# Performance work log

Measured on AMD Instinct MI355X. Metric: run time of the kernel, lower is better.

The kernel has to match this reference:

```python
import jax, jax.numpy as jnp
import numpy as np

B, TQ, TV, D = 32, 1024, 1024, 512


def setup_inputs() -> dict:
    key = jax.random.key(0)
    k1, k2, k3, k4 = jax.random.split(key, 4)
    scale = 1.0 / np.sqrt(D)
    return {
        "query": jax.random.normal(k1, (B, TQ, D), dtype=jnp.float32),
        "value": jax.random.normal(k2, (B, TV, D), dtype=jnp.float32),
        "w_weight": jax.random.normal(k3, (D, D), dtype=jnp.float32) * scale,
        "w_bias": jax.random.normal(k4, (D,), dtype=jnp.float32) * scale,
    }


def reference(query, value, w_weight, w_bias):
    # torch Linear: v @ W^T + b  -> keys [B, Tv, D]
    keys = jnp.einsum("bvd,ed->bve", value, w_weight) + w_bias
    # scores [B, Tq, Tv], softmax over Tv (last dim), unscaled as in source
    scores = jnp.einsum("bqd,bvd->bqv", query, keys)
    alignment = jax.nn.softmax(scores, axis=-1)
    context = jnp.einsum("bqv,bvd->bqd", alignment, value)
    context = jnp.concatenate([context, query], axis=-1)  # [B, Tq, 2D]
    alignment_t = jnp.swapaxes(alignment, 1, 2)  # [B, Tv, Tq]
    return context, alignment_t
```

## Files before the change

kernel.cpp:

```cpp
#include <hip/hip_runtime.h>
#include <hip/hip_bf16.h>

#define NB  32
#define NTQ 1024
#define NTV 1024
#define ND  512

typedef float f32x4 __attribute__((ext_vector_type(4)));
typedef float f32x2 __attribute__((ext_vector_type(2)));
typedef __bf16 bf16x8 __attribute__((ext_vector_type(8)));
typedef _Float16 f16x8 __attribute__((ext_vector_type(8)));
typedef unsigned short u16x4 __attribute__((ext_vector_type(4)));
typedef unsigned short u16x8 __attribute__((ext_vector_type(8)));
typedef unsigned int u32x2 __attribute__((ext_vector_type(2)));
typedef unsigned int u32x4 __attribute__((ext_vector_type(4)));

static __device__ __forceinline__ unsigned short f2h(float x) {
  _Float16 h = (_Float16)x;
  return __builtin_bit_cast(unsigned short, h);
}
static __device__ __forceinline__ float h2f(unsigned short u) {
  return (float)__builtin_bit_cast(_Float16, u);
}
static __device__ __forceinline__ unsigned split2(float x) {
  unsigned u = __builtin_bit_cast(unsigned, x);
  unsigned h = u >> 16;
  float hf = __builtin_bit_cast(float, u & 0xffff0000u);
  unsigned l = __builtin_bit_cast(unsigned, x - hf) >> 16;
  return h | (l << 16);
}
static __device__ __forceinline__ f32x4 mfma_bf(bf16x8 a, bf16x8 b, f32x4 c) {
  return __builtin_amdgcn_mfma_f32_16x16x32_bf16(a, b, c, 0, 0, 0);
}
static __device__ __forceinline__ f32x4 mfma_h(f16x8 a, f16x8 b, f32x4 c) {
  return __builtin_amdgcn_mfma_f32_16x16x32_f16(a, b, c, 0, 0, 0);
}
static __device__ __forceinline__ void gload16(const unsigned short* g, unsigned short* l) {
  __builtin_amdgcn_global_load_lds((const __attribute__((address_space(1))) unsigned*)g,
                                   (__attribute__((address_space(3))) unsigned*)l, 16, 0, 0);
}

__global__ __launch_bounds__(256) void k_vt(const float* __restrict__ V,
                                            unsigned short* __restrict__ Vt) {
  int vt = blockIdx.x, dt = blockIdx.y, b = blockIdx.z;
  int t = threadIdx.x;
  __shared__ unsigned short L[64][72];
#pragma unroll
  for (int r = 0; r < 4; ++r) {
    int v = (t >> 4) + r * 16;
    int c4 = (t & 15) * 4;
    f32x4 x = *(const f32x4*)(V + (size_t)(b * NTV + vt * 64 + v) * ND + dt * 64 + c4);
    u16x4 h;
#pragma unroll
    for (int j = 0; j < 4; ++j) h[j] = f2h(x[j]);
    *(u16x4*)&L[v][c4] = h;
  }
  __syncthreads();
#pragma unroll
  for (int r = 0; r < 4; ++r) {
    int d = (t >> 4) + r * 16;
    int v4 = (t & 15) * 4;
    u16x4 o;
#pragma unroll
    for (int i = 0; i < 4; ++i) o[i] = L[v4 + i][d];
    *(u16x4*)(Vt + (size_t)(b * ND + dt * 64 + d) * NTV + vt * 64 + v4) = o;
  }
}

__global__ __launch_bounds__(256) void k_qhalf(const float* __restrict__ Q,
                                               unsigned short* __restrict__ qh) {
  int base = blockIdx.x * 1024 + threadIdx.x;
#pragma unroll
  for (int k = 0; k < 4; ++k) {
    size_t c = (size_t)(base + k * 256) * 4;
    f32x4 x = *(const f32x4*)(Q + c);
    u16x4 h;
#pragma unroll
    for (int j = 0; j < 4; ++j) h[j] = f2h(x[j]);
    *(u16x4*)(qh + c) = h;
  }
}

__global__ __launch_bounds__(256, 2) void k_keys(const float* __restrict__ V,
                                                 const float* __restrict__ W,
                                                 const float* __restrict__ bias,
                                                 unsigned short* __restrict__ kp) {
  int bid = blockIdx.x;
  int swz = (bid & 7) * 128 + (bid >> 3);
  int bm = swz >> 2, bn = swz & 3;
  int t = threadIdx.x, lane = t & 63, w = t >> 6;
  int l15 = lane & 15, g = lane >> 4;
  int wr = (w >> 1) * 64, wc = (w & 1) * 64;
  __shared__ __align__(16) unsigned char SMEM[73728];
  auto Ah = (unsigned short(*)[72])(SMEM);
  auto Al = (unsigned short(*)[72])(SMEM + 18432);
  auto Bh = (unsigned short(*)[72])(SMEM + 36864);
  auto Bl = (unsigned short(*)[72])(SMEM + 55296);
  f32x4 acc[4][4] = {};
  const int row0 = bm * 128, col0 = bn * 128;
  int srow = t >> 4, c4 = (t & 15) * 4;

  f32x4 vreg[8], wreg[8];
#pragma unroll
  for (int r = 0; r < 8; ++r) {
    vreg[r] = *(const f32x4*)(V + (size_t)(row0 + srow + r * 16) * ND + c4);
    wreg[r] = *(const f32x4*)(W + (size_t)(col0 + srow + r * 16) * ND + c4);
  }
  for (int k0 = 0; k0 < ND; k0 += 64) {
    __syncthreads();
#pragma unroll
    for (int r = 0; r < 8; ++r) {
      int row = srow + r * 16;
      u16x4 h, l;
#pragma unroll
      for (int j = 0; j < 4; ++j) {
        unsigned p = split2(vreg[r][j]);
        h[j] = (unsigned short)(p & 0xffffu); l[j] = (unsigned short)(p >> 16);
      }
      *(u16x4*)&Ah[row][c4] = h; *(u16x4*)&Al[row][c4] = l;
#pragma unroll
      for (int j = 0; j < 4; ++j) {
        unsigned p = split2(wreg[r][j]);
        h[j] = (unsigned short)(p & 0xffffu); l[j] = (unsigned short)(p >> 16);
      }
      *(u16x4*)&Bh[row][c4] = h; *(u16x4*)&Bl[row][c4] = l;
    }
    __syncthreads();
    if (k0 + 64 < ND) {
#pragma unroll
      for (int r = 0; r < 8; ++r) {
        vreg[r] = *(const f32x4*)(V + (size_t)(row0 + srow + r * 16) * ND + k0 + 64 + c4);
        wreg[r] = *(const f32x4*)(W + (size_t)(col0 + srow + r * 16) * ND + k0 + 64 + c4);
      }
    }
#pragma unroll
    for (int kk = 0; kk < 2; ++kk) {
      int kof = kk * 32 + g * 8;
      bf16x8 ah[4], al[4], bh[4], bl[4];
#pragma unroll
      for (int i = 0; i < 4; ++i) {
        int ra = wr + i * 16 + l15;
        ah[i] = *(const bf16x8*)&Ah[ra][kof];
        al[i] = *(const bf16x8*)&Al[ra][kof];
        int rb = wc + i * 16 + l15;
        bh[i] = *(const bf16x8*)&Bh[rb][kof];
        bl[i] = *(const bf16x8*)&Bl[rb][kof];
      }
#pragma unroll
      for (int i = 0; i < 4; ++i)
#pragma unroll
        for (int j = 0; j < 4; ++j) {
          acc[i][j] = mfma_bf(ah[i], bh[j], acc[i][j]);
          acc[i][j] = mfma_bf(ah[i], bl[j], acc[i][j]);
          acc[i][j] = mfma_bf(al[i], bh[j], acc[i][j]);
        }
    }
  }
  __syncthreads();
  float* CT = (float*)SMEM;
#pragma unroll
  for (int j = 0; j < 4; ++j) {
    int col_l = wc + j * 16 + l15;
    float bj = bias[col0 + col_l];
#pragma unroll
    for (int i = 0; i < 4; ++i) {
      int rb_l = wr + i * 16 + g * 4;
#pragma unroll
      for (int r = 0; r < 4; ++r) CT[(rb_l + r) * 132 + col_l] = acc[i][j][r] + bj;
    }
  }
  __syncthreads();
#pragma unroll
  for (int it = 0; it < 16; ++it) {
    int idx = it * 256 + t;
    int row = idx >> 5, cc = (idx & 31) * 4;
    f32x4 x = *(const f32x4*)&CT[row * 132 + cc];
    u16x4 h;
#pragma unroll
    for (int j = 0; j < 4; ++j) h[j] = f2h(x[j]);
    *(u16x4*)(kp + (size_t)(row0 + row) * 2048 + col0 + cc) = h;
  }
}

__global__ __launch_bounds__(256, 3) void k_scores(const unsigned short* __restrict__ qh,
                                                   const unsigned short* kp,
                                                   unsigned short* ebase,
                                                   float2* __restrict__ partials) {
  int bid = blockIdx.x;
  int swz = (bid & 7) * 256 + (bid >> 3);
  int b = swz >> 6, rr2 = swz & 63, vt = rr2 >> 3, qt = rr2 & 7;
  int t = threadIdx.x, lane = t & 63, w = t >> 6, g = lane >> 4, l15 = lane & 15;
  int wr = (w >> 1) * 64, wc = (w & 1) * 64;
  __shared__ __align__(16) unsigned char SMEM[36864];
  unsigned short* lds = (unsigned short*)SMEM;
  f32x4 acc[4][4] = {};
  const size_t qrow = (size_t)(b * NTQ + qt * 128);
  const size_t krow = (size_t)(b * NTV + vt * 128);
  int grow = lane >> 3;
  int gcg = lane & 7;

  for (int k0 = 0; k0 < ND; k0 += 64) {
    __syncthreads();
#pragma unroll
    for (int i = 0; i < 4; ++i) {
      int c = i * 4 + w;
      int row = c * 8 + grow;
      int scg = gcg ^ (row & 7);
      gload16(qh + (qrow + row) * 512 + k0 + scg * 8, lds + c * 512);
      gload16(kp + (krow + row) * 2048 + k0 + scg * 8, lds + 8192 + c * 512);
    }
    __syncthreads();
#pragma unroll
    for (int kk = 0; kk < 2; ++kk) {
      f16x8 af[4], bfr[4];
#pragma unroll
      for (int i = 0; i < 4; ++i) {
        int ra = wr + i * 16 + l15;
        int go = ((kk * 4 + g) ^ (ra & 7)) * 8;
        af[i] = *(const f16x8*)(lds + ra * 64 + go);
        int rb = wc + i * 16 + l15;
        int go2 = ((kk * 4 + g) ^ (rb & 7)) * 8;
        bfr[i] = *(const f16x8*)(lds + 8192 + rb * 64 + go2);
      }
#pragma unroll
      for (int i = 0; i < 4; ++i)
#pragma unroll
        for (int j = 0; j < 4; ++j) acc[i][j] = mfma_h(af[i], bfr[j], acc[i][j]);
    }
  }
  __syncthreads();
  auto E2 = (unsigned short(*)[136])(SMEM);
  float* Lm = (float*)(SMEM + 34816);
  float* Ls = (float*)(SMEM + 35840);
#pragma unroll
  for (int i = 0; i < 4; ++i)
#pragma unroll
    for (int r = 0; r < 4; ++r) {
      float m = fmaxf(fmaxf(acc[i][0][r], acc[i][1][r]), fmaxf(acc[i][2][r], acc[i][3][r]));
#pragma unroll
      for (int msk = 1; msk < 16; msk <<= 1) m = fmaxf(m, __shfl_xor(m, msk));
      if (l15 == 0) Lm[(wr + i * 16 + g * 4 + r) * 2 + (w & 1)] = m;
    }
  __syncthreads();
#pragma unroll
  for (int i = 0; i < 4; ++i)
#pragma unroll
    for (int r = 0; r < 4; ++r) {
      int ql = wr + i * 16 + g * 4 + r;
      float mf = fmaxf(Lm[ql * 2], Lm[ql * 2 + 1]);
      float s = 0.f;
#pragma unroll
      for (int j = 0; j < 4; ++j) {
        float e = __expf(acc[i][j][r] - mf);
        s += e;
        E2[ql][wc + j * 16 + l15] = f2h(e);
      }
#pragma unroll
      for (int msk = 1; msk < 16; msk <<= 1) s += __shfl_xor(s, msk);
      if (l15 == 0) Ls[ql * 2 + (w & 1)] = s;
    }
  __syncthreads();
  if (t < 128) {
    float mf = fmaxf(Lm[t * 2], Lm[t * 2 + 1]);
    float lf = Ls[t * 2] + Ls[t * 2 + 1];
    partials[(((size_t)(b * 8 + vt)) << 10) + qt * 128 + t] = make_float2(mf, lf);
  }
#pragma unroll
  for (int it = 0; it < 8; ++it) {
    int idx = it * 256 + t;
    int row = idx >> 4, ch = idx & 15;
    *(u16x8*)(ebase + (size_t)(b * 1024 + qt * 128 + row) * 2048 + 1024 + vt * 128 + ch * 8) =
        *(const u16x8*)&E2[row][ch * 8];
  }
}

__global__ __launch_bounds__(256) void k_combine(const float2* __restrict__ partials,
                                                 float2* __restrict__ stats) {
  int idx = blockIdx.x * 256 + threadIdx.x;
  int b = idx >> 10, q = idx & 1023;
  float2 p[8];
  float M = -3.0e38f;
#pragma unroll
  for (int vt = 0; vt < 8; ++vt) {
    p[vt] = partials[(((size_t)(b * 8 + vt)) << 10) + q];
    M = fmaxf(M, p[vt].x);
  }
  float L = 0.f;
#pragma unroll
  for (int vt = 0; vt < 8; ++vt) L += p[vt].y * __expf(p[vt].x - M);
  stats[idx] = make_float2(M, 1.0f / L);
}

__global__ __launch_bounds__(256, 3) void k_pv(const unsigned short* __restrict__ ebase,
                                               const unsigned short* __restrict__ Vt,
                                               const float2* __restrict__ stats,
                                               const float2* __restrict__ partials,
                                               float* __restrict__ out1) {
  int bid = blockIdx.x;
  int swz = (bid & 7) * 128 + (bid >> 3);
  int b = swz >> 5, qt = (swz >> 2) & 7, dt = swz & 3;
  int t = threadIdx.x, lane = t & 63, w = t >> 6;
  int l15 = lane & 15, g = lane >> 4;
  int wr = (w >> 1) * 64, wc = (w & 1) * 64;
  int q0 = qt * 128, d0 = dt * 128;
  __shared__ __align__(16) unsigned char SMEM[36864];
  auto Ae = (unsigned short(*)[72])(SMEM);
  auto Bv = (unsigned short(*)[72])(SMEM + 18432);
  f32x4 acc[4][4] = {};

  int srow = t >> 3, c8 = (t & 7) * 8;
  float M4[4], iL4[4];
#pragma unroll
  for (int k = 0; k < 4; ++k) {
    float2 st = stats[b * NTQ + q0 + srow + 32 * k];
    M4[k] = st.x; iL4[k] = st.y;
  }
  u16x8 ereg[4], vreg[4];
#pragma unroll
  for (int k = 0; k < 4; ++k) {
    ereg[k] = *(const u16x8*)(ebase + (size_t)(b * 1024 + q0 + srow + 32 * k) * 2048 + 1024 + c8);
    vreg[k] = *(const u16x8*)(Vt + ((size_t)b * ND + d0 + srow + 32 * k) * NTV + c8);
  }
  float sck[4];
  for (int v0 = 0; v0 < NTV; v0 += 64) {
    if ((v0 & 127) == 0) {
      int vt128 = v0 >> 7;
#pragma unroll
      for (int k = 0; k < 4; ++k) {
        float2 p = partials[(((size_t)(b * 8 + vt128)) << 10) + q0 + srow + 32 * k];
        sck[k] = __expf(p.x - M4[k]) * iL4[k];
      }
    }
    __syncthreads();
#pragma unroll
    for (int k = 0; k < 4; ++k) {
      int row = srow + 32 * k;
      u16x8 a;
#pragma unroll
      for (int m = 0; m < 8; ++m) a[m] = f2h(h2f(ereg[k][m]) * sck[k]);
      *(u16x8*)&Ae[row][c8] = a;
      *(u16x8*)&Bv[row][c8] = vreg[k];
    }
    if (v0 + 64 < NTV) {
#pragma unroll
      for (int k = 0; k < 4; ++k) {
        ereg[k] = *(const u16x8*)(ebase + (size_t)(b * 1024 + q0 + srow + 32 * k) * 2048 + 1024 + v0 + 64 + c8);
        vreg[k] = *(const u16x8*)(Vt + ((size_t)b * ND + d0 + srow + 32 * k) * NTV + v0 + 64 + c8);
      }
    }
    __syncthreads();
#pragma unroll
    for (int kk = 0; kk < 2; ++kk) {
      int kof = kk * 32 + g * 8;
      f16x8 af[4], bfr[4];
#pragma unroll
      for (int i = 0; i < 4; ++i) af[i] = *(const f16x8*)&Ae[wr + i * 16 + l15][kof];
#pragma unroll
      for (int j = 0; j < 4; ++j) bfr[j] = *(const f16x8*)&Bv[wc + j * 16 + l15][kof];
#pragma unroll
      for (int i = 0; i < 4; ++i)
#pragma unroll
        for (int j = 0; j < 4; ++j) acc[i][j] = mfma_h(af[i], bfr[j], acc[i][j]);
    }
  }
  float* CT = (float*)SMEM;
#pragma unroll
  for (int h = 0; h < 2; ++h) {
    __syncthreads();
    if ((w >> 1) == h) {
#pragma unroll
      for (int i = 0; i < 4; ++i)
#pragma unroll
        for (int j = 0; j < 4; ++j) {
          int ql = i * 16 + g * 4;
          int dl = wc + j * 16 + l15;
#pragma unroll
          for (int r = 0; r < 4; ++r) CT[(ql + r) * 132 + dl] = acc[i][j][r];
        }
    }
    __syncthreads();
#pragma unroll
    for (int it = 0; it < 8; ++it) {
      int idx = it * 256 + t;
      int row = idx >> 5, c4 = idx & 31;
      *(f32x4*)(out1 + (size_t)(b * NTQ + q0 + h * 64 + row) * 1024 + d0 + c4 * 4) =
          *(const f32x4*)&CT[row * 132 + c4 * 4];
    }
  }
}

__global__ __launch_bounds__(256) void k_alpha(const unsigned short* ebase,
                                               const float* __restrict__ Q,
                                               const float2* __restrict__ stats,
                                               const float2* __restrict__ partials,
                                               float* out2,
                                               float* out1) {
  int bid = blockIdx.x;
  int swz = (bid & 7) * 64 + (bid >> 3);
  int b = swz >> 4, qc = swz & 15;
  int q0 = qc * 64;
  int t = threadIdx.x;
  __shared__ float T[128][68];
  int row = t >> 4, ch = t & 15;
  float M4[4], iL4[4];
#pragma unroll
  for (int k = 0; k < 4; ++k) {
    float2 st = stats[b * NTQ + q0 + row + 16 * k];
    M4[k] = st.x; iL4[k] = st.y;
  }
  for (int vt = 0; vt < 8; ++vt) {
    __syncthreads();
#pragma unroll
    for (int k = 0; k < 4; ++k) {
      int r = row + 16 * k;
      float2 p = partials[(((size_t)(b * 8 + vt)) << 10) + q0 + r];
      float sc = __expf(p.x - M4[k]) * iL4[k];
      u16x8 ev = *(const u16x8*)(ebase + (size_t)(b * 1024 + q0 + r) * 2048 + 1024 + vt * 128 + ch * 8);
#pragma unroll
      for (int m = 0; m < 8; ++m) {
        int v = ch * 8 + m;
        T[v][r ^ (((v >> 3) & 7) << 3)] = h2f(ev[m]) * sc;
      }
    }
    __syncthreads();
#pragma unroll
    for (int it = 0; it < 8; ++it) {
      int idx = it * 256 + t;
      int vr = idx >> 4, c4 = idx & 15;
      int cs = (c4 * 4) ^ (((vr >> 3) & 7) << 3);
      *(f32x4*)(out2 + ((size_t)(b * 1024) + vt * 128 + vr) * 1024 + q0 + c4 * 4) =
          *(const f32x4*)&T[vr][cs];
    }
  }
  __syncthreads();
#pragma unroll
  for (int k = 0; k < 32; ++k) {
    int idx = k * 256 + t;
    int r = idx >> 7, c4 = idx & 127;
    *(f32x4*)(out1 + (size_t)(b * 1024 + q0 + r) * 1024 + 512 + c4 * 4) =
        *(const f32x4*)(Q + (size_t)(b * 1024 + q0 + r) * 512 + c4 * 4);
  }
}

extern "C" void kernel_launch(void* const* d_in, const int* in_sizes, int n_in,
                              void* d_out, int out_size, void* d_ws, size_t ws_size,
                              hipStream_t stream) {
  const float* Q    = (const float*)d_in[0];
  const float* V    = (const float*)d_in[1];
  const float* W    = (const float*)d_in[2];
  const float* bias = (const float*)d_in[3];

  float* out1 = (float*)d_out;
  float* out2 = (float*)d_out + (size_t)NB * NTQ * (2 * ND);

  unsigned short* Vt = (unsigned short*)d_ws;
  float2* stats    = (float2*)((char*)d_ws + 33554432);
  float2* partials = (float2*)((char*)d_ws + 33554432 + 262144);

  unsigned short* kp = (unsigned short*)out1;
  unsigned short* ebase = (unsigned short*)out1;
  unsigned short* qh = (unsigned short*)out2;

  k_vt<<<dim3(16, 8, 32), 256, 0, stream>>>(V, Vt);
  k_qhalf<<<4096, 256, 0, stream>>>(Q, qh);
  k_keys<<<1024, 256, 0, stream>>>(V, W, bias, kp);
  k_scores<<<2048, 256, 0, stream>>>(qh, kp, ebase, partials);
  k_combine<<<128, 256, 0, stream>>>(partials, stats);
  k_pv<<<1024, 256, 0, stream>>>(ebase, Vt, stats, partials, out1);
  k_alpha<<<512, 256, 0, stream>>>(ebase, Q, stats, partials, out2, out1);
}
```

Before: 276.0 us.

## Merge prep kernels, pre-split W once, and stream W/Vt tiles via direct LDS loads

Merges the V-transpose and Q-to-half conversions into one prep kernel, which also pre-splits W into bf16 hi/lo arrays in the workspace. k_keys then loads the W tiles straight into LDS with global_load_lds using an XOR-swizzled layout, so each block no longer repeats the split and register staging. k_pv loads its Vt tiles the same way. This removes a launch, the redundant per-block W conversion and register pressure from staging. In exchange it adds extra workspace traffic and changes the LDS layout.

```diff
diff --git a/kernel.cpp b/kernel.cpp
--- a/kernel.cpp
+++ b/kernel.cpp
@@ -40,49 +40,70 @@
                                    (__attribute__((address_space(3))) unsigned*)l, 16, 0, 0);
 }
 
-__global__ __launch_bounds__(256) void k_vt(const float* __restrict__ V,
-                                            unsigned short* __restrict__ Vt) {
-  int vt = blockIdx.x, dt = blockIdx.y, b = blockIdx.z;
-  int t = threadIdx.x;
+__global__ __launch_bounds__(256) void k_prep(const float* __restrict__ V,
+                                              const float* __restrict__ Q,
+                                              const float* __restrict__ W,
+                                              unsigned short* __restrict__ Vt,
+                                              unsigned short* __restrict__ qh,
+                                              unsigned short* __restrict__ wh,
+                                              unsigned short* __restrict__ wl) {
   __shared__ unsigned short L[64][72];
-#pragma unroll
-  for (int r = 0; r < 4; ++r) {
-    int v = (t >> 4) + r * 16;
-    int c4 = (t & 15) * 4;
-    f32x4 x = *(const f32x4*)(V + (size_t)(b * NTV + vt * 64 + v) * ND + dt * 64 + c4);
-    u16x4 h;
-#pragma unroll
-    for (int j = 0; j < 4; ++j) h[j] = f2h(x[j]);
-    *(u16x4*)&L[v][c4] = h;
-  }
-  __syncthreads();
-#pragma unroll
-  for (int r = 0; r < 4; ++r) {
-    int d = (t >> 4) + r * 16;
-    int v4 = (t & 15) * 4;
-    u16x4 o;
-#pragma unroll
-    for (int i = 0; i < 4; ++i) o[i] = L[v4 + i][d];
-    *(u16x4*)(Vt + (size_t)(b * ND + dt * 64 + d) * NTV + vt * 64 + v4) = o;
-  }
-}
-
-__global__ __launch_bounds__(256) void k_qhalf(const float* __restrict__ Q,
-                                               unsigned short* __restrict__ qh) {
-  int base = blockIdx.x * 1024 + threadIdx.x;
-#pragma unroll
-  for (int k = 0; k < 4; ++k) {
-    size_t c = (size_t)(base + k * 256) * 4;
-    f32x4 x = *(const f32x4*)(Q + c);
-    u16x4 h;
-#pragma unroll
-    for (int j = 0; j < 4; ++j) h[j] = f2h(x[j]);
-    *(u16x4*)(qh + c) = h;
+  int bid = blockIdx.x, t = threadIdx.x;
+  if (bid < 4096) {
+    int vt = bid & 15, dt = (bid >> 4) & 7, b = bid >> 7;
+#pragma unroll
+    for (int r = 0; r < 4; ++r) {
+      int v = (t >> 4) + r * 16;
+      int c4 = (t & 15) * 4;
+      f32x4 x = *(const f32x4*)(V + (size_t)(b * NTV + vt * 64 + v) * ND + dt * 64 + c4);
+      u16x4 h;
+#pragma unroll
+      for (int j = 0; j < 4; ++j) h[j] = f2h(x[j]);
+      *(u16x4*)&L[v][c4] = h;
+    }
+    __syncthreads();
+#pragma unroll
+    for (int r = 0; r < 4; ++r) {
+      int d = (t >> 4) + r * 16;
+      int v4 = (t & 15) * 4;
+      u16x4 o;
+#pragma unroll
+      for (int i = 0; i < 4; ++i) o[i] = L[v4 + i][d];
+      *(u16x4*)(Vt + (size_t)(b * ND + dt * 64 + d) * NTV + vt * 64 + v4) = o;
+    }
+  } else if (bid < 8192) {
+    int base = (bid - 4096) * 1024 + t;
+#pragma unroll
+    for (int k = 0; k < 4; ++k) {
+      size_t c = (size_t)(base + k * 256) * 4;
+      f32x4 x = *(const f32x4*)(Q + c);
+      u16x4 h;
+#pragma unroll
+      for (int j = 0; j < 4; ++j) h[j] = f2h(x[j]);
+      *(u16x4*)(qh + c) = h;
+    }
+  } else {
+    int base = (bid - 8192) * 1024 + t;
+#pragma unroll
+    for (int k = 0; k < 4; ++k) {
+      size_t c = (size_t)(base + k * 256) * 4;
+      f32x4 x = *(const f32x4*)(W + c);
+      u16x4 hi, lo;
+#pragma unroll
+      for (int j = 0; j < 4; ++j) {
+        unsigned p = split2(x[j]);
+        hi[j] = (unsigned short)(p & 0xffffu);
+        lo[j] = (unsigned short)(p >> 16);
+      }
+      *(u16x4*)(wh + c) = hi;
+      *(u16x4*)(wl + c) = lo;
+    }
   }
 }
 
 __global__ __launch_bounds__(256, 2) void k_keys(const float* __restrict__ V,
-                                                 const float* __restrict__ W,
+                                                 const unsigned short* wh,
+                                                 const unsigned short* wl,
                                                  const float* __restrict__ bias,
                                                  unsigned short* __restrict__ kp) {
   int bid = blockIdx.x;
@@ -91,23 +112,31 @@
   int t = threadIdx.x, lane = t & 63, w = t >> 6;
   int l15 = lane & 15, g = lane >> 4;
   int wr = (w >> 1) * 64, wc = (w & 1) * 64;
-  __shared__ __align__(16) unsigned char SMEM[73728];
+  __shared__ __align__(16) unsigned char SMEM[69632];
   auto Ah = (unsigned short(*)[72])(SMEM);
   auto Al = (unsigned short(*)[72])(SMEM + 18432);
-  auto Bh = (unsigned short(*)[72])(SMEM + 36864);
-  auto Bl = (unsigned short(*)[72])(SMEM + 55296);
+  unsigned short* ldsBh = (unsigned short*)(SMEM + 36864);
+  unsigned short* ldsBl = (unsigned short*)(SMEM + 53248);
   f32x4 acc[4][4] = {};
   const int row0 = bm * 128, col0 = bn * 128;
   int srow = t >> 4, c4 = (t & 15) * 4;
-
-  f32x4 vreg[8], wreg[8];
-#pragma unroll
-  for (int r = 0; r < 8; ++r) {
+  int grow = lane >> 3, gcg = lane & 7;
+
+  f32x4 vreg[8];
+#pragma unroll
+  for (int r = 0; r < 8; ++r)
     vreg[r] = *(const f32x4*)(V + (size_t)(row0 + srow + r * 16) * ND + c4);
-    wreg[r] = *(const f32x4*)(W + (size_t)(col0 + srow + r * 16) * ND + c4);
-  }
+
   for (int k0 = 0; k0 < ND; k0 += 64) {
     __syncthreads();
+#pragma unroll
+    for (int i = 0; i < 4; ++i) {
+      int c = i * 4 + w;
+      int row = c * 8 + grow;
+      int scg = gcg ^ (row & 7);
+      gload16(wh + (size_t)(col0 + row) * 512 + k0 + scg * 8, ldsBh + c * 512);
+      gload16(wl + (size_t)(col0 + row) * 512 + k0 + scg * 8, ldsBl + c * 512);
+    }
 #pragma unroll
     for (int r = 0; r < 8; ++r) {
       int row = srow + r * 16;
@@ -118,20 +147,12 @@
         h[j] = (unsigned short)(p & 0xffffu); l[j] = (unsigned short)(p >> 16);
       }
       *(u16x4*)&Ah[row][c4] = h; *(u16x4*)&Al[row][c4] = l;
-#pragma unroll
-      for (int j = 0; j < 4; ++j) {
-        unsigned p = split2(wreg[r][j]);
-        h[j] = (unsigned short)(p & 0xffffu); l[j] = (unsigned short)(p >> 16);
-      }
-      *(u16x4*)&Bh[row][c4] = h; *(u16x4*)&Bl[row][c4] = l;
     }
     __syncthreads();
     if (k0 + 64 < ND) {
 #pragma unroll
-      for (int r = 0; r < 8; ++r) {
+      for (int r = 0; r < 8; ++r)
         vreg[r] = *(const f32x4*)(V + (size_t)(row0 + srow + r * 16) * ND + k0 + 64 + c4);
-        wreg[r] = *(const f32x4*)(W + (size_t)(col0 + srow + r * 16) * ND + k0 + 64 + c4);
-      }
     }
 #pragma unroll
     for (int kk = 0; kk < 2; ++kk) {
@@ -143,8 +164,9 @@
         ah[i] = *(const bf16x8*)&Ah[ra][kof];
         al[i] = *(const bf16x8*)&Al[ra][kof];
         int rb = wc + i * 16 + l15;
-        bh[i] = *(const bf16x8*)&Bh[rb][kof];
-        bl[i] = *(const bf16x8*)&Bl[rb][kof];
+        int go2 = ((kk * 4 + g) ^ (rb & 7)) * 8;
+        bh[i] = *(const bf16x8*)(ldsBh + rb * 64 + go2);
+        bl[i] = *(const bf16x8*)(ldsBl + rb * 64 + go2);
       }
 #pragma unroll
       for (int i = 0; i < 4; ++i)
@@ -196,8 +218,7 @@
   f32x4 acc[4][4] = {};
   const size_t qrow = (size_t)(b * NTQ + qt * 128);
   const size_t krow = (size_t)(b * NTV + vt * 128);
-  int grow = lane >> 3;
-  int gcg = lane & 7;
+  int grow = lane >> 3, gcg = lane & 7;
 
   for (int k0 = 0; k0 < ND; k0 += 64) {
     __syncthreads();
@@ -292,7 +313,7 @@
 }
 
 __global__ __launch_bounds__(256, 3) void k_pv(const unsigned short* __restrict__ ebase,
-                                               const unsigned short* __restrict__ Vt,
+                                               const unsigned short* Vt,
                                                const float2* __restrict__ stats,
                                                const float2* __restrict__ partials,
                                                float* __restrict__ out1) {
@@ -305,22 +326,22 @@
   int q0 = qt * 128, d0 = dt * 128;
   __shared__ __align__(16) unsigned char SMEM[36864];
   auto Ae = (unsigned short(*)[72])(SMEM);
-  auto Bv = (unsigned short(*)[72])(SMEM + 18432);
+  unsigned short* ldsBv = (unsigned short*)(SMEM + 18432);
   f32x4 acc[4][4] = {};
 
   int srow = t >> 3, c8 = (t & 7) * 8;
+  int grow = lane >> 3, gcg = lane & 7;
   float M4[4], iL4[4];
 #pragma unroll
   for (int k = 0; k < 4; ++k) {
     float2 st = stats[b * NTQ + q0 + srow + 32 * k];
     M4[k] = st.x; iL4[k] = st.y;
   }
-  u16x8 ereg[4], vreg[4];
-#pragma unroll
-  for (int k = 0; k < 4; ++k) {
+  u16x8 ereg[4];
+#pragma unroll
+  for (int k = 0; k < 4; ++k)
     ereg[k] = *(const u16x8*)(ebase + (size_t)(b * 1024 + q0 + srow + 32 * k) * 2048 + 1024 + c8);
-    vreg[k] = *(const u16x8*)(Vt + ((size_t)b * ND + d0 + srow + 32 * k) * NTV + c8);
-  }
+
   float sck[4];
   for (int v0 = 0; v0 < NTV; v0 += 64) {
     if ((v0 & 127) == 0) {
@@ -333,20 +354,24 @@
     }
     __syncthreads();
 #pragma unroll
+    for (int i = 0; i < 4; ++i) {
+      int c = i * 4 + w;
+      int row = c * 8 + grow;
+      int scg = gcg ^ (row & 7);
+      gload16(Vt + ((size_t)b * ND + d0 + row) * NTV + v0 + scg * 8, ldsBv + c * 512);
+    }
+#pragma unroll
     for (int k = 0; k < 4; ++k) {
       int row = srow + 32 * k;
       u16x8 a;
 #pragma unroll
       for (int m = 0; m < 8; ++m) a[m] = f2h(h2f(ereg[k][m]) * sck[k]);
       *(u16x8*)&Ae[row][c8] = a;
-      *(u16x8*)&Bv[row][c8] = vreg[k];
     }
     if (v0 + 64 < NTV) {
 #pragma unroll
-      for (int k = 0; k < 4; ++k) {
+      for (int k = 0; k < 4; ++k)
         ereg[k] = *(const u16x8*)(ebase + (size_t)(b * 1024 + q0 + srow + 32 * k) * 2048 + 1024 + v0 + 64 + c8);
-        vreg[k] = *(const u16x8*)(Vt + ((size_t)b * ND + d0 + srow + 32 * k) * NTV + v0 + 64 + c8);
-      }
     }
     __syncthreads();
 #pragma unroll
@@ -356,7 +381,11 @@
 #pragma unroll
       for (int i = 0; i < 4; ++i) af[i] = *(const f16x8*)&Ae[wr + i * 16 + l15][kof];
 #pragma unroll
-      for (int j = 0; j < 4; ++j) bfr[j] = *(const f16x8*)&Bv[wc + j * 16 + l15][kof];
+      for (int j = 0; j < 4; ++j) {
+        int rb = wc + j * 16 + l15;
+        int go2 = ((kk * 4 + g) ^ (rb & 7)) * 8;
+        bfr[j] = *(const f16x8*)(ldsBv + rb * 64 + go2);
+      }
 #pragma unroll
       for (int i = 0; i < 4; ++i)
 #pragma unroll
@@ -456,14 +485,15 @@
   unsigned short* Vt = (unsigned short*)d_ws;
   float2* stats    = (float2*)((char*)d_ws + 33554432);
   float2* partials = (float2*)((char*)d_ws + 33554432 + 262144);
+  unsigned short* wh = (unsigned short*)((char*)d_ws + 35913728);
+  unsigned short* wl = (unsigned short*)((char*)d_ws + 36438016);
 
   unsigned short* kp = (unsigned short*)out1;
   unsigned short* ebase = (unsigned short*)out1;
   unsigned short* qh = (unsigned short*)out2;
 
-  k_vt<<<dim3(16, 8, 32), 256, 0, stream>>>(V, Vt);
-  k_qhalf<<<4096, 256, 0, stream>>>(Q, qh);
-  k_keys<<<1024, 256, 0, stream>>>(V, W, bias, kp);
+  k_prep<<<8256, 256, 0, stream>>>(V, Q, W, Vt, qh, wh, wl);
+  k_keys<<<1024, 256, 0, stream>>>(V, wh, wl, bias, kp);
   k_scores<<<2048, 256, 0, stream>>>(qh, kp, ebase, partials);
   k_combine<<<128, 256, 0, stream>>>(partials, stats);
   k_pv<<<1024, 256, 0, stream>>>(ebase, Vt, stats, partials, out1);
```

New measurement: 286.1 us. 1.04x slower.
